# Kernel optimization log

Measured on AMD Instinct MI355X. Metric: run time of the kernel, lower is better.

Reference implementation:

```python
import jax, jax.numpy as jnp
import numpy as np

N, E = 50000, 1600000
DIM_IN, HEADS, DIM_OUT = 256, 4, 32
NEG_SLOPE = 0.2


def setup_inputs() -> dict:
    key = jax.random.key(0)
    k1, k2, k3, k4, k5, k6 = jax.random.split(key, 6)
    x = jax.random.normal(k1, (N, DIM_IN), dtype=jnp.float32)
    edge_index = jax.random.randint(k2, (2, E), 0, N, dtype=jnp.int64)
    s = 1.0 / np.sqrt(DIM_IN)
    W = jax.random.normal(k3, (DIM_IN, HEADS * DIM_OUT), dtype=jnp.float32) * s
    att_src = jax.random.normal(k4, (HEADS, DIM_OUT), dtype=jnp.float32) * 0.1
    att_dst = jax.random.normal(k5, (HEADS, DIM_OUT), dtype=jnp.float32) * 0.1
    bias = jax.random.normal(k6, (HEADS * DIM_OUT,), dtype=jnp.float32) * 0.01
    return {"x": x, "edge_index": edge_index, "W": W,
            "att_src": att_src, "att_dst": att_dst, "bias": bias}


def reference(x, edge_index, W, att_src, att_dst, bias):
    n = x.shape[0]
    h, c = att_src.shape
    # linear projection, per-head view [N, H, C]
    xp = (x @ W).reshape(n, h, c)
    # per-node attention logits [N, H]
    a_src = jnp.einsum('nhc,hc->nh', xp, att_src)
    a_dst = jnp.einsum('nhc,hc->nh', xp, att_dst)
    # add self loops (PyG default add_self_loops=True)
    loops = jnp.arange(n, dtype=edge_index.dtype)
    src = jnp.concatenate([edge_index[0], loops])  # [E+N]
    dst = jnp.concatenate([edge_index[1], loops])
    # edge attention scores [E+N, H]
    e = jax.nn.leaky_relu(a_src[src] + a_dst[dst], negative_slope=NEG_SLOPE)
    # segment softmax over incoming edges of each dst node
    emax = jax.ops.segment_max(e, dst, num_segments=n)
    ex = jnp.exp(e - emax[dst])
    denom = jax.ops.segment_sum(ex, dst, num_segments=n)
    alpha = ex / denom[dst]  # [E+N, H]
    # weighted scatter-aggregate of src features
    msg = xp[src] * alpha[:, :, None]  # [E+N, H, C]
    out = jax.ops.segment_sum(msg, dst, num_segments=n)  # [N, H, C]
    return out.reshape(n, h * c) + bias
```

## Files before the change

kernel.cpp:

```cpp
#include <hip/hip_runtime.h>
#include <hip/hip_fp16.h>


#define DIN 256
#define HC 128
#define NH 4
#define NEG 0.2f
#define BSH 8
#define BSZ 256

typedef _Float16 half8 __attribute__((ext_vector_type(8)));
typedef _Float16 half2v __attribute__((ext_vector_type(2)));
typedef float f32x4 __attribute__((ext_vector_type(4)));

__global__ void zero_kernel(int* __restrict__ p, int n) {
    int i = blockIdx.x * blockDim.x + threadIdx.x;
    if (i < n) p[i] = 0;
}

__global__ __launch_bounds__(256) void wtrans_kernel(const float* __restrict__ W,
                                                     _Float16* __restrict__ Wt) {
    int i = blockIdx.x * 256 + threadIdx.x;
    int k = i >> 7, c = i & 127;
    Wt[c * 256 + k] = (_Float16)W[i];
}

__global__ __launch_bounds__(256) void proj_kernel(const float* __restrict__ x,
                                                   const _Float16* __restrict__ Wt,
                                                   const float* __restrict__ attS,
                                                   const float* __restrict__ attD,
                                                   __half* __restrict__ xph,
                                                   float* __restrict__ a_src,
                                                   float* __restrict__ a_dst, int n) {
    __shared__ _Float16 smem[8704];
    __shared__ float attSL[128], attDL[128];
    _Float16* xs = smem;
    _Float16* Wl = smem + 2560;
    _Float16* ep = smem;

    const int tid  = threadIdx.x;
    const int node0 = blockIdx.x * 64;
    const int wave = tid >> 6;
    const int lane = tid & 63;
    const int l15  = lane & 15;
    const int quad = lane >> 4;

    if (tid < 128) attSL[tid] = attS[tid];
    else           attDL[tid - 128] = attD[tid - 128];

    f32x4 acc[8];
#pragma unroll
    for (int ct = 0; ct < 8; ++ct) acc[ct] = (f32x4){0.f, 0.f, 0.f, 0.f};

    for (int kt = 0; kt < DIN; kt += 32) {
        __syncthreads();
#pragma unroll
        for (int r = 0; r < 4; ++r) {
            int idx = tid + r * 256;
            int row = idx >> 4;
            int kp  = idx & 15;
            int gn = node0 + row;
            float2 xv = make_float2(0.f, 0.f);
            if (gn < n) xv = *(const float2*)&x[(size_t)gn * DIN + kt + kp * 2];
            half2v p; p[0] = (_Float16)xv.x; p[1] = (_Float16)xv.y;
            *(half2v*)&xs[row * 40 + kp * 2] = p;
        }
#pragma unroll
        for (int r = 0; r < 2; ++r) {
            int id = tid + r * 256;
            int c = id >> 2;
            int q = id & 3;
            half8 wv = *(const half8*)&Wt[(size_t)c * 256 + kt + q * 8];
            *(half8*)&Wl[c * 40 + q * 8] = wv;
        }
        __syncthreads();
        half8 af = *(const half8*)&xs[(wave * 16 + l15) * 40 + quad * 8];
#pragma unroll
        for (int ct = 0; ct < 8; ++ct) {
            half8 bf = *(const half8*)&Wl[(ct * 16 + l15) * 40 + quad * 8];
            acc[ct] = __builtin_amdgcn_mfma_f32_16x16x32_f16(af, bf, acc[ct], 0, 0, 0);
        }
    }
    __syncthreads();
#pragma unroll
    for (int ct = 0; ct < 8; ++ct)
#pragma unroll
        for (int r = 0; r < 4; ++r) {
            int row = wave * 16 + quad * 4 + r;
            ep[row * 136 + ct * 16 + l15] = (_Float16)acc[ct][r];
        }
    __syncthreads();
    {
        int row = tid >> 2, ch = tid & 3;
        int node = node0 + row;
        if (node < n) {
            const uint4* s = (const uint4*)&ep[row * 136 + ch * 32];
            uint4* d = (uint4*)&xph[(size_t)node * HC + ch * 32];
            d[0] = s[0]; d[1] = s[1]; d[2] = s[2]; d[3] = s[3];
        }
    }
    {
        int nl = tid >> 2, h = tid & 3;
        int node = node0 + nl;
        if (node < n) {
            float ps = 0.f, pd = 0.f;
            const _Float16* er = &ep[nl * 136 + h * 32];
#pragma unroll
            for (int c = 0; c < 32; ++c) {
                float v = (float)er[c];
                ps += v * attSL[h * 32 + c];
                pd += v * attDL[h * 32 + c];
            }
            a_src[node * NH + h] = ps;
            a_dst[node * NH + h] = pd;
        }
    }
}

__global__ __launch_bounds__(256) void hist_kernel(const int* __restrict__ ei,
                                                   int* __restrict__ ghist, int e, int n) {
    __shared__ int h[256];
    const int tid = threadIdx.x;
    h[tid] = 0;
    __syncthreads();
    const int base = blockIdx.x * 4096;
#pragma unroll
    for (int j = 0; j < 16; ++j) {
        int i = base + j * 256 + tid;
        if (i < e) {
            int src = ei[i];
            int dst = ei[e + i];
            if ((unsigned)dst < (unsigned)n && (unsigned)src < (unsigned)n)
                atomicAdd(&h[dst >> BSH], 1);
        }
    }
    __syncthreads();
    if (h[tid]) atomicAdd(&ghist[tid], h[tid]);
}

__global__ __launch_bounds__(256) void bscan_kernel(const int* __restrict__ ghist,
                                                    int* __restrict__ gbase,
                                                    int* __restrict__ gcur, int nbuck) {
    __shared__ int buf[256];
    const int tid = threadIdx.x;
    int v = (tid < nbuck) ? ghist[tid] : 0;
    buf[tid] = v;
    __syncthreads();
    for (int s = 1; s < 256; s <<= 1) {
        int t = (tid >= s) ? buf[tid - s] : 0;
        __syncthreads();
        buf[tid] += t;
        __syncthreads();
    }
    int excl = buf[tid] - v;
    if (tid < nbuck) { gbase[tid] = excl; gcur[tid] = excl; }
    if (tid == nbuck - 1) gbase[nbuck] = buf[tid];
}

__global__ __launch_bounds__(256) void bin_kernel(const int* __restrict__ ei,
                                                  int* __restrict__ gcur,
                                                  unsigned* __restrict__ binned,
                                                  int e, int n) {
    __shared__ int h[256];
    __shared__ int rbase[256];
    const int tid = threadIdx.x;
    h[tid] = 0;
    __syncthreads();
    const int base = blockIdx.x * 4096;
    unsigned pk[16];
    int bk[16];
#pragma unroll
    for (int j = 0; j < 16; ++j) {
        int i = base + j * 256 + tid;
        bk[j] = -1;
        if (i < e) {
            int src = ei[i];
            int dst = ei[e + i];
            if ((unsigned)dst < (unsigned)n && (unsigned)src < (unsigned)n) {
                bk[j] = dst >> BSH;
                pk[j] = ((unsigned)(dst & (BSZ - 1)) << 24) | (unsigned)src;
                atomicAdd(&h[bk[j]], 1);
            }
        }
    }
    __syncthreads();
    if (h[tid]) rbase[tid] = atomicAdd(&gcur[tid], h[tid]);
    h[tid] = 0;
    __syncthreads();
#pragma unroll
    for (int j = 0; j < 16; ++j) {
        if (bk[j] >= 0) {
            int p = atomicAdd(&h[bk[j]], 1);
            binned[rbase[bk[j]] + p] = pk[j];
        }
    }
}

__global__ __launch_bounds__(256) void csr_kernel(const unsigned* __restrict__ binned,
                                                  const int* __restrict__ gbase,
                                                  const float* __restrict__ a_src,
                                                  const float* __restrict__ a_dst,
                                                  int* __restrict__ off,
                                                  int* __restrict__ srt,
                                                  __half* __restrict__ escore,
                                                  int n, int nbuck) {
    __shared__ int cnt[256], buf[256], cur[256];
    __shared__ float adL[BSZ * 4];
    const int tid = threadIdx.x;
    const int b = blockIdx.x;
    const int kb = gbase[b];
    const int ke = gbase[b + 1];
    cnt[tid] = 0;
#pragma unroll
    for (int r = 0; r < 4; ++r) {
        int idx = tid + r * 256;
        int gi = b * (BSZ * 4) + idx;
        adL[idx] = (gi < n * 4) ? a_dst[gi] : 0.f;
    }
    __syncthreads();
    for (int i = kb + tid; i < ke; i += 256)
        atomicAdd(&cnt[binned[i] >> 24], 1);
    __syncthreads();
    int v = cnt[tid];
    buf[tid] = v;
    __syncthreads();
    for (int s = 1; s < 256; s <<= 1) {
        int t = (tid >= s) ? buf[tid - s] : 0;
        __syncthreads();
        buf[tid] += t;
        __syncthreads();
    }
    const int excl = kb + buf[tid] - v;
    const int node = b * BSZ + tid;
    if (node < n) off[node] = excl;
    if (tid == 0 && b == nbuck - 1) off[n] = ke;
    cur[tid] = excl;
    __syncthreads();
    for (int i = kb + tid; i < ke; i += 256) {
        unsigned pv = binned[i];
        int nl = pv >> 24;
        int src = (int)(pv & 0xFFFFFFu);
        int pos = atomicAdd(&cur[nl], 1);
        srt[pos] = src;
        const float4 asv = *(const float4*)&a_src[(size_t)src * 4];
        float t0 = asv.x + adL[nl * 4 + 0]; t0 = (t0 > 0.f) ? t0 : NEG * t0;
        float t1 = asv.y + adL[nl * 4 + 1]; t1 = (t1 > 0.f) ? t1 : NEG * t1;
        float t2 = asv.z + adL[nl * 4 + 2]; t2 = (t2 > 0.f) ? t2 : NEG * t2;
        float t3 = asv.w + adL[nl * 4 + 3]; t3 = (t3 > 0.f) ? t3 : NEG * t3;
        __half2* epr = (__half2*)&escore[(size_t)pos * 4];
        epr[0] = __floats2half2_rn(__expf(t0), __expf(t1));
        epr[1] = __floats2half2_rn(__expf(t2), __expf(t3));
    }
}

__global__ __launch_bounds__(256) void agg_kernel(const __half2* __restrict__ xh2,
                                                  const float* __restrict__ a_src,
                                                  const float* __restrict__ a_dst,
                                                  const int* __restrict__ off,
                                                  const int* __restrict__ srt,
                                                  const __half* __restrict__ escore,
                                                  const float* __restrict__ bias,
                                                  float* __restrict__ out, int n) {
    const int gwave = (blockIdx.x * blockDim.x + threadIdx.x) >> 6;
    if (gwave >= n) return;
    const int node = gwave;
    const int lane = threadIdx.x & 63;
    const int h = lane >> 4;

    float e0 = a_src[node * NH + h] + a_dst[node * NH + h];
    e0 = (e0 > 0.f) ? e0 : NEG * e0;
    float g = __expf(e0);
    float2 v = __half22float2(xh2[(size_t)node * 64 + lane]);
    float accx = g * v.x, accy = g * v.y, den = g;

    const int kb = off[node];
    const int ke = off[node + 1];
    int k = kb;
    for (; k + 8 <= ke; k += 8) {
        int s[8];
#pragma unroll
        for (int j = 0; j < 8; ++j) s[j] = srt[k + j];
        float sc[8];
#pragma unroll
        for (int j = 0; j < 8; ++j) sc[j] = __half2float(escore[(size_t)(k + j) * 4 + h]);
        __half2 hv[8];
#pragma unroll
        for (int j = 0; j < 8; ++j) hv[j] = xh2[(size_t)s[j] * 64 + lane];
#pragma unroll
        for (int j = 0; j < 8; ++j) {
            float2 vf = __half22float2(hv[j]);
            accx += sc[j] * vf.x;
            accy += sc[j] * vf.y;
            den  += sc[j];
        }
    }
    for (; k < ke; ++k) {
        const int s = srt[k];
        const float sc = __half2float(escore[(size_t)k * 4 + h]);
        const float2 vf = __half22float2(xh2[(size_t)s * 64 + lane]);
        accx += sc * vf.x;
        accy += sc * vf.y;
        den  += sc;
    }
    const float2 b2 = ((const float2*)bias)[lane];
    const float inv = 1.0f / den;
    float2 o;
    o.x = accx * inv + b2.x;
    o.y = accy * inv + b2.y;
    ((float2*)out)[(size_t)node * 64 + lane] = o;
}

extern "C" void kernel_launch(void* const* d_in, const int* in_sizes, int n_in,
                              void* d_out, int out_size, void* d_ws, size_t ws_size,
                              hipStream_t stream) {
    if (n_in < 6 || !d_out || !d_ws) return;
    const float* x    = (const float*)d_in[0];
    const int*   ei   = (const int*)d_in[1];
    const float* W    = (const float*)d_in[2];
    const float* attS = (const float*)d_in[3];
    const float* attD = (const float*)d_in[4];
    const float* bias = (const float*)d_in[5];
    float* out = (float*)d_out;

    const int N = in_sizes[0] / DIN;
    const int E = in_sizes[1] / 2;
    if (N <= 0 || E <= 0) return;
    const int NBUCK = (N + BSZ - 1) >> BSH;
    if (NBUCK > 256 || N > (1 << 24)) return;

    char* ws = (char*)d_ws;
    size_t off_b = 0;
    auto carve = [&](size_t bytes) {
        size_t p = off_b;
        off_b = (off_b + bytes + 255) & ~(size_t)255;
        return (void*)(ws + p);
    };
    __half*    xph    = (__half*)carve((size_t)N * HC * 2);
    _Float16*  Wt     = (_Float16*)carve((size_t)HC * DIN * 2);
    float*     a_src  = (float*)carve((size_t)N * NH * 4);
    float*     a_dst  = (float*)carve((size_t)N * NH * 4);
    int*       ghist  = (int*)carve(257 * 4);
    int*       gbase  = (int*)carve(257 * 4);
    int*       gcur   = (int*)carve(257 * 4);
    unsigned*  binned = (unsigned*)carve((size_t)E * 4);
    int*       offp   = (int*)carve((size_t)(N + 1) * 4);
    int*       srt    = (int*)carve((size_t)E * 4);
    __half*    escore = (__half*)carve((size_t)E * NH * 2);
    (void)out_size;
    if (off_b > ws_size) return;

    const int ECH = (E + 4095) / 4096;

    zero_kernel<<<2, 256, 0, stream>>>(ghist, 257);
    wtrans_kernel<<<(DIN * HC) / 256, 256, 0, stream>>>(W, Wt);
    proj_kernel<<<(N + 63) / 64, 256, 0, stream>>>(x, Wt, attS, attD, xph, a_src, a_dst, N);
    hist_kernel<<<ECH, 256, 0, stream>>>(ei, ghist, E, N);
    bscan_kernel<<<1, 256, 0, stream>>>(ghist, gbase, gcur, NBUCK);
    bin_kernel<<<ECH, 256, 0, stream>>>(ei, gcur, binned, E, N);
    csr_kernel<<<NBUCK, 256, 0, stream>>>(binned, gbase, a_src, a_dst, offp, srt,
                                          escore, N, NBUCK);
    agg_kernel<<<(N * 64 + 255) / 256, 256, 0, stream>>>((const __half2*)xph, a_src, a_dst,
                                                         offp, srt, escore, bias, out, N);
}
```

Before: 262.5 us.

## Split edge-score computation out of CSR kernel into fully parallel escore kernel

Removes the exp/leaky-relu edge score computation from the csr_kernel, which runs only NBUCK (~196) blocks, and moves it into a new kernel with one thread per edge. Sorted entries now pack dst in the high 16 bits and src in the low 16 bits so the new kernel can recover both endpoints. The intent is to relieve the low-parallelism CSR pass, which was doing random a_src gathers. In exchange it adds a kernel launch and an extra pass over srt, limits N to 65536, and drops the src bounds check in the histogram kernel.

```diff
diff --git a/kernel.cpp b/kernel.cpp
--- a/kernel.cpp
+++ b/kernel.cpp
@@ -128,10 +128,8 @@
     for (int j = 0; j < 16; ++j) {
         int i = base + j * 256 + tid;
         if (i < e) {
-            int src = ei[i];
             int dst = ei[e + i];
-            if ((unsigned)dst < (unsigned)n && (unsigned)src < (unsigned)n)
-                atomicAdd(&h[dst >> BSH], 1);
+            if ((unsigned)dst < (unsigned)n) atomicAdd(&h[dst >> BSH], 1);
         }
     }
     __syncthreads();
@@ -198,25 +196,15 @@
 
 __global__ __launch_bounds__(256) void csr_kernel(const unsigned* __restrict__ binned,
                                                   const int* __restrict__ gbase,
-                                                  const float* __restrict__ a_src,
-                                                  const float* __restrict__ a_dst,
                                                   int* __restrict__ off,
-                                                  int* __restrict__ srt,
-                                                  __half* __restrict__ escore,
+                                                  unsigned* __restrict__ srt,
                                                   int n, int nbuck) {
     __shared__ int cnt[256], buf[256], cur[256];
-    __shared__ float adL[BSZ * 4];
     const int tid = threadIdx.x;
     const int b = blockIdx.x;
     const int kb = gbase[b];
     const int ke = gbase[b + 1];
     cnt[tid] = 0;
-#pragma unroll
-    for (int r = 0; r < 4; ++r) {
-        int idx = tid + r * 256;
-        int gi = b * (BSZ * 4) + idx;
-        adL[idx] = (gi < n * 4) ? a_dst[gi] : 0.f;
-    }
     __syncthreads();
     for (int i = kb + tid; i < ke; i += 256)
         atomicAdd(&cnt[binned[i] >> 24], 1);
@@ -236,28 +224,42 @@
     if (tid == 0 && b == nbuck - 1) off[n] = ke;
     cur[tid] = excl;
     __syncthreads();
+    const unsigned dbase = (unsigned)(b * BSZ) << 16;
     for (int i = kb + tid; i < ke; i += 256) {
         unsigned pv = binned[i];
         int nl = pv >> 24;
-        int src = (int)(pv & 0xFFFFFFu);
         int pos = atomicAdd(&cur[nl], 1);
-        srt[pos] = src;
-        const float4 asv = *(const float4*)&a_src[(size_t)src * 4];
-        float t0 = asv.x + adL[nl * 4 + 0]; t0 = (t0 > 0.f) ? t0 : NEG * t0;
-        float t1 = asv.y + adL[nl * 4 + 1]; t1 = (t1 > 0.f) ? t1 : NEG * t1;
-        float t2 = asv.z + adL[nl * 4 + 2]; t2 = (t2 > 0.f) ? t2 : NEG * t2;
-        float t3 = asv.w + adL[nl * 4 + 3]; t3 = (t3 > 0.f) ? t3 : NEG * t3;
-        __half2* epr = (__half2*)&escore[(size_t)pos * 4];
-        epr[0] = __floats2half2_rn(__expf(t0), __expf(t1));
-        epr[1] = __floats2half2_rn(__expf(t2), __expf(t3));
-    }
+        srt[pos] = (dbase + ((unsigned)nl << 16)) | (pv & 0xFFFFu);
+    }
+}
+
+__global__ __launch_bounds__(256) void escore_kernel(const unsigned* __restrict__ srt,
+                                                     const float* __restrict__ a_src,
+                                                     const float* __restrict__ a_dst,
+                                                     __half* __restrict__ escore,
+                                                     int e, int n) {
+    int i = blockIdx.x * 256 + threadIdx.x;
+    if (i >= e) return;
+    unsigned v = srt[i];
+    int src = (int)(v & 0xFFFFu);
+    int dst = (int)(v >> 16);
+    if (src >= n || dst >= n) return;
+    const float4 as = *(const float4*)&a_src[(size_t)src * 4];
+    const float4 ad = *(const float4*)&a_dst[(size_t)dst * 4];
+    float t0 = as.x + ad.x; t0 = (t0 > 0.f) ? t0 : NEG * t0;
+    float t1 = as.y + ad.y; t1 = (t1 > 0.f) ? t1 : NEG * t1;
+    float t2 = as.z + ad.z; t2 = (t2 > 0.f) ? t2 : NEG * t2;
+    float t3 = as.w + ad.w; t3 = (t3 > 0.f) ? t3 : NEG * t3;
+    __half2* ep = (__half2*)&escore[(size_t)i * 4];
+    ep[0] = __floats2half2_rn(__expf(t0), __expf(t1));
+    ep[1] = __floats2half2_rn(__expf(t2), __expf(t3));
 }
 
 __global__ __launch_bounds__(256) void agg_kernel(const __half2* __restrict__ xh2,
                                                   const float* __restrict__ a_src,
                                                   const float* __restrict__ a_dst,
                                                   const int* __restrict__ off,
-                                                  const int* __restrict__ srt,
+                                                  const unsigned* __restrict__ srt,
                                                   const __half* __restrict__ escore,
                                                   const float* __restrict__ bias,
                                                   float* __restrict__ out, int n) {
@@ -279,7 +281,7 @@
     for (; k + 8 <= ke; k += 8) {
         int s[8];
 #pragma unroll
-        for (int j = 0; j < 8; ++j) s[j] = srt[k + j];
+        for (int j = 0; j < 8; ++j) s[j] = (int)(srt[k + j] & 0xFFFFu);
         float sc[8];
 #pragma unroll
         for (int j = 0; j < 8; ++j) sc[j] = __half2float(escore[(size_t)(k + j) * 4 + h]);
@@ -295,7 +297,7 @@
         }
     }
     for (; k < ke; ++k) {
-        const int s = srt[k];
+        const int s = (int)(srt[k] & 0xFFFFu);
         const float sc = __half2float(escore[(size_t)k * 4 + h]);
         const float2 vf = __half22float2(xh2[(size_t)s * 64 + lane]);
         accx += sc * vf.x;
@@ -326,7 +328,7 @@
     const int E = in_sizes[1] / 2;
     if (N <= 0 || E <= 0) return;
     const int NBUCK = (N + BSZ - 1) >> BSH;
-    if (NBUCK > 256 || N > (1 << 24)) return;
+    if (NBUCK > 256 || N > 65536) return;
 
     char* ws = (char*)d_ws;
     size_t off_b = 0;
@@ -344,7 +346,7 @@
     int*       gcur   = (int*)carve(257 * 4);
     unsigned*  binned = (unsigned*)carve((size_t)E * 4);
     int*       offp   = (int*)carve((size_t)(N + 1) * 4);
-    int*       srt    = (int*)carve((size_t)E * 4);
+    unsigned*  srt    = (unsigned*)carve((size_t)E * 4);
     __half*    escore = (__half*)carve((size_t)E * NH * 2);
     (void)out_size;
     if (off_b > ws_size) return;
@@ -357,8 +359,8 @@
     hist_kernel<<<ECH, 256, 0, stream>>>(ei, ghist, E, N);
     bscan_kernel<<<1, 256, 0, stream>>>(ghist, gbase, gcur, NBUCK);
     bin_kernel<<<ECH, 256, 0, stream>>>(ei, gcur, binned, E, N);
-    csr_kernel<<<NBUCK, 256, 0, stream>>>(binned, gbase, a_src, a_dst, offp, srt,
-                                          escore, N, NBUCK);
+    csr_kernel<<<NBUCK, 256, 0, stream>>>(binned, gbase, offp, srt, N, NBUCK);
+    escore_kernel<<<(E + 255) / 256, 256, 0, stream>>>(srt, a_src, a_dst, escore, E, N);
     agg_kernel<<<(N * 64 + 255) / 256, 256, 0, stream>>>((const __half2*)xph, a_src, a_dst,
                                                          offp, srt, escore, bias, out, N);
 }
```

Result: faster. 253.3 us (-3.5%).
